# Performance work log

Measured on AMD Instinct MI355X. Metric: run time of the kernel, lower is better.

## Reference

```python
import jax, jax.numpy as jnp
import numpy as np

EPS = 1e-8

def setup_inputs() -> dict:
    key = jax.random.key(0)
    k1, k2 = jax.random.split(key)
    B, C, H, W = 8, 21, 512, 512
    inp = jax.random.normal(k1, (B, C, H, W), dtype=jnp.float32)
    target = jax.random.uniform(k2, (B, C, H, W), dtype=jnp.float32)
    return {"input": inp, "target": target}

def reference(input, target):
    B, C, H, W = input.shape
    # argmax over class dim -> [B, H, W]
    pred = jnp.argmax(input, axis=1)
    # one-hot of prediction, flattened over spatial dims -> [B, HW, C]
    h = jax.nn.one_hot(pred.reshape(B, H * W), C, dtype=input.dtype)
    # target flattened over spatial dims -> [B, C, HW]
    y = target.reshape(B, C, H * W)
    # cm[b, i, j] = sum_n y[b, i, n] * h[b, n, j]  -> [B, C, C]
    cm = jnp.einsum('bin,bnj->bij', y, h)
    # row-normalize by target mass per class, then mean over batch -> [C, C]
    cm = cm / (jnp.sum(y, axis=2, keepdims=True) + EPS)
    return jnp.mean(cm, axis=0)
```

## Files before the change

kernel.cpp:

```cpp
#include <hip/hip_runtime.h>

#define NC 21
#define NB 8
#define HW (512*512)
#define EPS 1e-8f
#define NREP 8

__global__ __launch_bounds__(256) void cm_accum(const float* __restrict__ input,
                                                const float* __restrict__ target,
                                                float* __restrict__ cm ) {
    __shared__ float scm[NREP][NC * NC];
    const int t = threadIdx.x;
    for (int i = t; i < NREP * NC * NC; i += 256) ((float*)scm)[i] = 0.0f;
    __syncthreads();

    const int b    = blockIdx.x >> 8;
    const int tile = blockIdx.x & 255;
    const int q    = (tile << 8) + t;

    const float4* ip = (const float4*)(input  + (size_t)b * NC * HW);
    const float4* tp = (const float4*)(target + (size_t)b * NC * HW);
    const int plane4 = HW / 4;

    float4 v[NC];
    #pragma unroll
    for (int c = 0; c < NC; ++c) v[c] = ip[c * plane4 + q];
    __builtin_amdgcn_sched_barrier(0);

    float4 m = v[0];
    int jx = 0, jy = 0, jz = 0, jw = 0;
    #pragma unroll
    for (int c = 1; c < NC; ++c) {
        if (v[c].x > m.x) { m.x = v[c].x; jx = c; }
        if (v[c].y > m.y) { m.y = v[c].y; jy = c; }
        if (v[c].z > m.z) { m.z = v[c].z; jz = c; }
        if (v[c].w > m.w) { m.w = v[c].w; jw = c; }
    }

    float4 y[NC];
    #pragma unroll
    for (int c = 0; c < NC; ++c) y[c] = tp[c * plane4 + q];
    __builtin_amdgcn_sched_barrier(0);

    float* my = scm[t & (NREP - 1)];
    #pragma unroll
    for (int c = 0; c < NC; ++c) {
        const int row = c * NC;
        atomicAdd(&my[row + jx], y[c].x);
        atomicAdd(&my[row + jy], y[c].y);
        atomicAdd(&my[row + jz], y[c].z);
        atomicAdd(&my[row + jw], y[c].w);
    }
    __syncthreads();

    for (int i = t; i < NC * NC; i += 256) {
        float s = 0.0f;
        #pragma unroll
        for (int r = 0; r < NREP; ++r) s += scm[r][i];
        atomicAdd(&cm[b * NC * NC + i], s);
    }
}

__global__ __launch_bounds__(512) void cm_final(const float* __restrict__ cm,
                                                float* __restrict__ out) {
    __shared__ float rs[NB * NC];
    const int t = threadIdx.x;
    if (t < NB * NC) {
        const int b = t / NC, i = t % NC;
        float s = 0.0f;
        for (int j = 0; j < NC; ++j) s += cm[b * NC * NC + i * NC + j];
        rs[t] = s + EPS;
    }
    __syncthreads();
    if (t < NC * NC) {
        const int i = t / NC;
        float acc = 0.0f;
        for (int b = 0; b < NB; ++b) acc += cm[b * NC * NC + t] / rs[b * NC + i];
        out[t] = acc * (1.0f / NB);
    }
}

extern "C" void kernel_launch(void* const* d_in, const int* in_sizes, int n_in,
                              void* d_out, int out_size, void* d_ws, size_t ws_size,
                              hipStream_t stream) {
    const float* input  = (const float*)d_in[0];
    const float* target = (const float*)d_in[1];
    float* out = (float*)d_out;
    float* cm  = (float*)d_ws;

    hipMemsetAsync(cm, 0, NB * NC * NC * sizeof(float), stream);
    cm_accum<<<NB * 256, 256, 0, stream>>>(input, target, cm);
    cm_final<<<1, 512, 0, stream>>>(cm, out);
}
```

Before: 502.7 us.

## Replace global atomics with per-block partials plus reduce kernel; nontemporal loads

Each accumulation block now writes its 441-entry partial confusion matrix to a workspace slot instead of issuing global atomicAdds, and a new reduce kernel sums the 256 tiles per batch. This removes the memset and the contention on global atomics. The input loads also switch to nontemporal loads to avoid polluting the cache. The cost is an extra kernel launch and about 4 MB of partial writes and reads. When the workspace is too small, the code falls back to the old atomic path.

```diff
diff --git a/kernel.cpp b/kernel.cpp
--- a/kernel.cpp
+++ b/kernel.cpp
@@ -5,10 +5,17 @@
 #define HW (512*512)
 #define EPS 1e-8f
 #define NREP 8
+#define NTILE 256
+#define PSTRIDE 512
 
+typedef float f32x4 __attribute__((ext_vector_type(4)));
+
+
+template <bool PARTIAL>
 __global__ __launch_bounds__(256) void cm_accum(const float* __restrict__ input,
                                                 const float* __restrict__ target,
-                                                float* __restrict__ cm ) {
+                                                float* __restrict__ cm ,
+                                                float* __restrict__ partial ) {
     __shared__ float scm[NREP][NC * NC];
     const int t = threadIdx.x;
     for (int i = t; i < NREP * NC * NC; i += 256) ((float*)scm)[i] = 0.0f;
@@ -18,16 +25,16 @@
     const int tile = blockIdx.x & 255;
     const int q    = (tile << 8) + t;
 
-    const float4* ip = (const float4*)(input  + (size_t)b * NC * HW);
-    const float4* tp = (const float4*)(target + (size_t)b * NC * HW);
+    const f32x4* ip = (const f32x4*)(input  + (size_t)b * NC * HW);
+    const f32x4* tp = (const f32x4*)(target + (size_t)b * NC * HW);
     const int plane4 = HW / 4;
 
-    float4 v[NC];
+    f32x4 v[NC];
     #pragma unroll
-    for (int c = 0; c < NC; ++c) v[c] = ip[c * plane4 + q];
+    for (int c = 0; c < NC; ++c) v[c] = __builtin_nontemporal_load(ip + c * plane4 + q);
     __builtin_amdgcn_sched_barrier(0);
 
-    float4 m = v[0];
+    f32x4 m = v[0];
     int jx = 0, jy = 0, jz = 0, jw = 0;
     #pragma unroll
     for (int c = 1; c < NC; ++c) {
@@ -37,9 +44,9 @@
         if (v[c].w > m.w) { m.w = v[c].w; jw = c; }
     }
 
-    float4 y[NC];
+    f32x4 y[NC];
     #pragma unroll
-    for (int c = 0; c < NC; ++c) y[c] = tp[c * plane4 + q];
+    for (int c = 0; c < NC; ++c) y[c] = __builtin_nontemporal_load(tp + c * plane4 + q);
     __builtin_amdgcn_sched_barrier(0);
 
     float* my = scm[t & (NREP - 1)];
@@ -53,12 +60,38 @@
     }
     __syncthreads();
 
-    for (int i = t; i < NC * NC; i += 256) {
-        float s = 0.0f;
-        #pragma unroll
-        for (int r = 0; r < NREP; ++r) s += scm[r][i];
-        atomicAdd(&cm[b * NC * NC + i], s);
+    if (PARTIAL) {
+        float* pout = partial + (size_t)blockIdx.x * PSTRIDE;
+        for (int i = t; i < PSTRIDE; i += 256) {
+            float s = 0.0f;
+            if (i < NC * NC) {
+                #pragma unroll
+                for (int r = 0; r < NREP; ++r) s += scm[r][i];
+            }
+            pout[i] = s;
+        }
+    } else {
+        for (int i = t; i < NC * NC; i += 256) {
+            float s = 0.0f;
+            #pragma unroll
+            for (int r = 0; r < NREP; ++r) s += scm[r][i];
+            atomicAdd(&cm[b * NC * NC + i], s);
+        }
     }
+}
+
+__global__ __launch_bounds__(256) void cm_reduce(const float* __restrict__ partial,
+                                                 float* __restrict__ cm) {
+    const int b = blockIdx.x, t = threadIdx.x;
+    const float* p = partial + (size_t)b * NTILE * PSTRIDE;
+    float s0 = 0.0f, s1 = 0.0f;
+    #pragma unroll 8
+    for (int s = 0; s < NTILE; ++s) {
+        s0 += p[(size_t)s * PSTRIDE + t];
+        s1 += p[(size_t)s * PSTRIDE + t + 256];
+    }
+    cm[b * NC * NC + t] = s0;
+    if (t + 256 < NC * NC) cm[b * NC * NC + t + 256] = s1;
 }
 
 __global__ __launch_bounds__(512) void cm_final(const float* __restrict__ cm,
@@ -86,9 +119,20 @@
     const float* input  = (const float*)d_in[0];
     const float* target = (const float*)d_in[1];
     float* out = (float*)d_out;
-    float* cm  = (float*)d_ws;
 
-    hipMemsetAsync(cm, 0, NB * NC * NC * sizeof(float), stream);
-    cm_accum<<<NB * 256, 256, 0, stream>>>(input, target, cm);
-    cm_final<<<1, 512, 0, stream>>>(cm, out);
+    const size_t partial_floats = (size_t)NB * NTILE * PSTRIDE;
+    const size_t need = (partial_floats + NB * NC * NC) * sizeof(float);
+
+    if (ws_size >= need) {
+        float* partial = (float*)d_ws;
+        float* cm      = partial + partial_floats;
+        cm_accum<true><<<NB * NTILE, 256, 0, stream>>>(input, target, cm, partial);
+        cm_reduce<<<NB, 256, 0, stream>>>(partial, cm);
+        cm_final<<<1, 512, 0, stream>>>(cm, out);
+    } else {
+        float* cm = (float*)d_ws;
+        hipMemsetAsync(cm, 0, NB * NC * NC * sizeof(float), stream);
+        cm_accum<false><<<NB * NTILE, 256, 0, stream>>>(input, target, cm, nullptr);
+        cm_final<<<1, 512, 0, stream>>>(cm, out);
+    }
 }
```

New measurement: 514.8 us. 2.4% more time.
